# Kernel optimization log

Measured on AMD Instinct MI355X. Metric: run time of the kernel, lower is better.

## Reference

```python
import jax, jax.numpy as jnp
import numpy as np

B, T, D = 32, 2048, 512

def setup_inputs() -> dict:
    key = jax.random.key(0)
    k1, k2, k3 = jax.random.split(key, 3)
    return {
        "query": jax.random.normal(k1, (B, D), dtype=jnp.float32),
        "key": jax.random.normal(k2, (B, T, D), dtype=jnp.float32),
        "value": jax.random.normal(k3, (B, T, D), dtype=jnp.float32),
    }

def reference(query, key, value):
    # energy: [B, T] = bmm(key [B,T,D], query [B,D,1]).squeeze
    energy = jnp.einsum("btd,bd->bt", key, query)
    attention = jax.nn.softmax(energy, axis=1)  # over T, no scaling/masking (faithful)
    # context: [B, D] = bmm(attention [B,1,T], value [B,T,D]).squeeze
    out = jnp.einsum("bt,btd->bd", attention, value)
    return (out, attention)
```

## Files before the change

kernel.cpp:

```cpp
#include <hip/hip_runtime.h>

#define B_ 32
#define T_ 2048
#define D_ 512

__global__ __launch_bounds__(256) void energy_kernel(
    const float* __restrict__ q,
    const float* __restrict__ key,
    float* __restrict__ energy)
{
    __shared__ float4 qs[128];
    const int b = blockIdx.x >> 9;
    if (threadIdx.x < 128)
        qs[threadIdx.x] = ((const float4*)q)[b * 128 + threadIdx.x];
    __syncthreads();

    const int wave = threadIdx.x >> 6;
    const int lane = threadIdx.x & 63;
    const int gw   = blockIdx.x * 4 + wave;
    const int t    = gw & (T_ - 1);

    const float4* k4 = (const float4*)key + (size_t)(b * T_ + t) * (D_ / 4);
    float acc = 0.f;
#pragma unroll
    for (int j = 0; j < 2; ++j) {
        float4 kv = k4[j * 64 + lane];
        float4 qv = qs[j * 64 + lane];
        acc += kv.x * qv.x + kv.y * qv.y + kv.z * qv.z + kv.w * qv.w;
    }
#pragma unroll
    for (int off = 32; off >= 1; off >>= 1)
        acc += __shfl_down(acc, off);
    if (lane == 0)
        energy[gw] = acc;
}

__global__ __launch_bounds__(256) void softmax_kernel(
    const float* __restrict__ energy,
    float* __restrict__ attn)
{
    const int b = blockIdx.x;
    const int wave = threadIdx.x >> 6;
    const int lane = threadIdx.x & 63;

    const float4* e4 = (const float4*)(energy + b * T_);
    float4 v0 = e4[threadIdx.x * 2 + 0];
    float4 v1 = e4[threadIdx.x * 2 + 1];

    float m = fmaxf(fmaxf(fmaxf(v0.x, v0.y), fmaxf(v0.z, v0.w)),
                    fmaxf(fmaxf(v1.x, v1.y), fmaxf(v1.z, v1.w)));
#pragma unroll
    for (int off = 32; off >= 1; off >>= 1)
        m = fmaxf(m, __shfl_xor(m, off));
    __shared__ float redm[4];
    if (lane == 0) redm[wave] = m;
    __syncthreads();
    m = fmaxf(fmaxf(redm[0], redm[1]), fmaxf(redm[2], redm[3]));

    float4 x0, x1;
    x0.x = expf(v0.x - m); x0.y = expf(v0.y - m);
    x0.z = expf(v0.z - m); x0.w = expf(v0.w - m);
    x1.x = expf(v1.x - m); x1.y = expf(v1.y - m);
    x1.z = expf(v1.z - m); x1.w = expf(v1.w - m);
    float s = x0.x + x0.y + x0.z + x0.w + x1.x + x1.y + x1.z + x1.w;
#pragma unroll
    for (int off = 32; off >= 1; off >>= 1)
        s += __shfl_xor(s, off);
    __shared__ float reds[4];
    if (lane == 0) reds[wave] = s;
    __syncthreads();
    s = reds[0] + reds[1] + reds[2] + reds[3];

    const float inv = 1.f / s;
    x0.x *= inv; x0.y *= inv; x0.z *= inv; x0.w *= inv;
    x1.x *= inv; x1.y *= inv; x1.z *= inv; x1.w *= inv;

    float4* a4 = (float4*)(attn + b * T_);
    a4[threadIdx.x * 2 + 0] = x0;
    a4[threadIdx.x * 2 + 1] = x1;
}

__global__ __launch_bounds__(512) void context_partial_kernel(
    const float* __restrict__ attn,
    const float* __restrict__ value,
    float* __restrict__ partial)
{
    __shared__ float  attn_s[256];
    __shared__ float4 red4[512];

    const int b     = blockIdx.x >> 3;
    const int chunk = blockIdx.x & 7;
    const int t0    = chunk * 256;

    if (threadIdx.x < 256)
        attn_s[threadIdx.x] = attn[b * T_ + t0 + threadIdx.x];
    __syncthreads();

    const int tg = threadIdx.x >> 7;
    const int d4 = threadIdx.x & 127;

    const float4* v4 = (const float4*)value + (size_t)(b * T_ + t0 + tg) * (D_ / 4) + d4;
    float4 acc = {0.f, 0.f, 0.f, 0.f};
#pragma unroll 8
    for (int i = 0; i < 64; ++i) {
        const float a = attn_s[4 * i + tg];
        const float4 vv = v4[i * 4 * (D_ / 4)];
        acc.x += a * vv.x; acc.y += a * vv.y;
        acc.z += a * vv.z; acc.w += a * vv.w;
    }

    red4[tg * 128 + d4] = acc;
    __syncthreads();
    if (threadIdx.x < 128) {
        float4 a0 = red4[threadIdx.x +   0];
        float4 a1 = red4[threadIdx.x + 128];
        float4 a2 = red4[threadIdx.x + 256];
        float4 a3 = red4[threadIdx.x + 384];
        float4 sv;
        sv.x = a0.x + a1.x + a2.x + a3.x;
        sv.y = a0.y + a1.y + a2.y + a3.y;
        sv.z = a0.z + a1.z + a2.z + a3.z;
        sv.w = a0.w + a1.w + a2.w + a3.w;
        ((float4*)partial)[(b * 8 + chunk) * 128 + threadIdx.x] = sv;
    }
}

__global__ __launch_bounds__(128) void reduce_kernel(
    const float* __restrict__ partial,
    float* __restrict__ out)
{
    const int b  = blockIdx.x;
    const int d4 = threadIdx.x;
    float4 s = {0.f, 0.f, 0.f, 0.f};
#pragma unroll
    for (int c = 0; c < 8; ++c) {
        float4 p = ((const float4*)partial)[(b * 8 + c) * 128 + d4];
        s.x += p.x; s.y += p.y; s.z += p.z; s.w += p.w;
    }
    ((float4*)out)[b * 128 + d4] = s;
}

extern "C" void kernel_launch(void* const* d_in, const int* in_sizes, int n_in,
                              void* d_out, int out_size, void* d_ws, size_t ws_size,
                              hipStream_t stream)
{
    const float* q     = (const float*)d_in[0];
    const float* key   = (const float*)d_in[1];
    const float* value = (const float*)d_in[2];

    float* out  = (float*)d_out;
    float* attn = out + B_ * D_;

    float* energy  = (float*)d_ws;
    float* partial = energy + B_ * T_;

    energy_kernel<<<B_ * T_ / 4, 256, 0, stream>>>(q, key, energy);
    softmax_kernel<<<B_, 256, 0, stream>>>(energy, attn);
    context_partial_kernel<<<B_ * 8, 512, 0, stream>>>(attn, value, partial);
    reduce_kernel<<<B_, 128, 0, stream>>>(partial, out);
}
```

Baseline: 277.6 us.

## Rebalance energy and context kernels: more rows per wave, more context blocks

The energy kernel now has each wave handle 8 key rows, holding the query in registers instead of shared memory and dropping the block barrier, so far fewer blocks are launched. The context kernel splits T into 32 chunks of 64 with 256-thread blocks, giving 1024 blocks instead of 256 to fill more CUs while streaming value. The reduce kernel then sums 32 partials per batch instead of 8. Softmax switches to fast __expf, trading a little accuracy for cheaper exponentials.

```diff
diff --git a/kernel.cpp b/kernel.cpp
--- a/kernel.cpp
+++ b/kernel.cpp
@@ -9,30 +9,29 @@
     const float* __restrict__ key,
     float* __restrict__ energy)
 {
-    __shared__ float4 qs[128];
-    const int b = blockIdx.x >> 9;
-    if (threadIdx.x < 128)
-        qs[threadIdx.x] = ((const float4*)q)[b * 128 + threadIdx.x];
-    __syncthreads();
-
+    const int b    = blockIdx.x >> 6;
+    const int t0   = (blockIdx.x & 63) * 32;
     const int wave = threadIdx.x >> 6;
     const int lane = threadIdx.x & 63;
-    const int gw   = blockIdx.x * 4 + wave;
-    const int t    = gw & (T_ - 1);
 
-    const float4* k4 = (const float4*)key + (size_t)(b * T_ + t) * (D_ / 4);
-    float acc = 0.f;
+    const float4 qv0 = ((const float4*)q)[b * 128 + lane];
+    const float4 qv1 = ((const float4*)q)[b * 128 + 64 + lane];
+
+    const int trow = t0 + wave * 8;
+    const float4* kbase = (const float4*)key + ((size_t)b * T_ + trow) * 128;
+
+#pragma unroll 4
+    for (int r = 0; r < 8; ++r) {
+        const float4 k0 = kbase[r * 128 + lane];
+        const float4 k1 = kbase[r * 128 + 64 + lane];
+        float acc = k0.x * qv0.x + k0.y * qv0.y + k0.z * qv0.z + k0.w * qv0.w
+                  + k1.x * qv1.x + k1.y * qv1.y + k1.z * qv1.z + k1.w * qv1.w;
 #pragma unroll
-    for (int j = 0; j < 2; ++j) {
-        float4 kv = k4[j * 64 + lane];
-        float4 qv = qs[j * 64 + lane];
-        acc += kv.x * qv.x + kv.y * qv.y + kv.z * qv.z + kv.w * qv.w;
+        for (int off = 32; off >= 1; off >>= 1)
+            acc += __shfl_down(acc, off);
+        if (lane == 0)
+            energy[b * T_ + trow + r] = acc;
     }
-#pragma unroll
-    for (int off = 32; off >= 1; off >>= 1)
-        acc += __shfl_down(acc, off);
-    if (lane == 0)
-        energy[gw] = acc;
 }
 
 __global__ __launch_bounds__(256) void softmax_kernel(
@@ -58,10 +57,10 @@
     m = fmaxf(fmaxf(redm[0], redm[1]), fmaxf(redm[2], redm[3]));
 
     float4 x0, x1;
-    x0.x = expf(v0.x - m); x0.y = expf(v0.y - m);
-    x0.z = expf(v0.z - m); x0.w = expf(v0.w - m);
-    x1.x = expf(v1.x - m); x1.y = expf(v1.y - m);
-    x1.z = expf(v1.z - m); x1.w = expf(v1.w - m);
+    x0.x = __expf(v0.x - m); x0.y = __expf(v0.y - m);
+    x0.z = __expf(v0.z - m); x0.w = __expf(v0.w - m);
+    x1.x = __expf(v1.x - m); x1.y = __expf(v1.y - m);
+    x1.z = __expf(v1.z - m); x1.w = __expf(v1.w - m);
     float s = x0.x + x0.y + x0.z + x0.w + x1.x + x1.y + x1.z + x1.w;
 #pragma unroll
     for (int off = 32; off >= 1; off >>= 1)
@@ -80,48 +79,41 @@
     a4[threadIdx.x * 2 + 1] = x1;
 }
 
-__global__ __launch_bounds__(512) void context_partial_kernel(
+__global__ __launch_bounds__(256) void context_partial_kernel(
     const float* __restrict__ attn,
     const float* __restrict__ value,
     float* __restrict__ partial)
 {
-    __shared__ float  attn_s[256];
-    __shared__ float4 red4[512];
+    __shared__ float  attn_s[64];
+    __shared__ float4 red4[128];
 
-    const int b     = blockIdx.x >> 3;
-    const int chunk = blockIdx.x & 7;
-    const int t0    = chunk * 256;
+    const int b     = blockIdx.x >> 5;
+    const int chunk = blockIdx.x & 31;
+    const int t0    = chunk * 64;
 
-    if (threadIdx.x < 256)
+    if (threadIdx.x < 64)
         attn_s[threadIdx.x] = attn[b * T_ + t0 + threadIdx.x];
     __syncthreads();
 
     const int tg = threadIdx.x >> 7;
     const int d4 = threadIdx.x & 127;
 
-    const float4* v4 = (const float4*)value + (size_t)(b * T_ + t0 + tg) * (D_ / 4) + d4;
+    const float4* v4 = (const float4*)value + ((size_t)b * T_ + t0 + tg) * 128 + d4;
     float4 acc = {0.f, 0.f, 0.f, 0.f};
 #pragma unroll 8
-    for (int i = 0; i < 64; ++i) {
-        const float a = attn_s[4 * i + tg];
-        const float4 vv = v4[i * 4 * (D_ / 4)];
+    for (int i = 0; i < 32; ++i) {
+        const float a = attn_s[2 * i + tg];
+        const float4 vv = v4[i * 256];
         acc.x += a * vv.x; acc.y += a * vv.y;
         acc.z += a * vv.z; acc.w += a * vv.w;
     }
 
-    red4[tg * 128 + d4] = acc;
+    if (tg == 1) red4[d4] = acc;
     __syncthreads();
-    if (threadIdx.x < 128) {
-        float4 a0 = red4[threadIdx.x +   0];
-        float4 a1 = red4[threadIdx.x + 128];
-        float4 a2 = red4[threadIdx.x + 256];
-        float4 a3 = red4[threadIdx.x + 384];
-        float4 sv;
-        sv.x = a0.x + a1.x + a2.x + a3.x;
-        sv.y = a0.y + a1.y + a2.y + a3.y;
-        sv.z = a0.z + a1.z + a2.z + a3.z;
-        sv.w = a0.w + a1.w + a2.w + a3.w;
-        ((float4*)partial)[(b * 8 + chunk) * 128 + threadIdx.x] = sv;
+    if (tg == 0) {
+        const float4 o = red4[d4];
+        acc.x += o.x; acc.y += o.y; acc.z += o.z; acc.w += o.w;
+        ((float4*)partial)[((size_t)b * 32 + chunk) * 128 + d4] = acc;
     }
 }
 
@@ -133,8 +125,8 @@
     const int d4 = threadIdx.x;
     float4 s = {0.f, 0.f, 0.f, 0.f};
 #pragma unroll
-    for (int c = 0; c < 8; ++c) {
-        float4 p = ((const float4*)partial)[(b * 8 + c) * 128 + d4];
+    for (int c = 0; c < 32; ++c) {
+        const float4 p = ((const float4*)partial)[((size_t)b * 32 + c) * 128 + d4];
         s.x += p.x; s.y += p.y; s.z += p.z; s.w += p.w;
     }
     ((float4*)out)[b * 128 + d4] = s;
@@ -154,8 +146,8 @@
     float* energy  = (float*)d_ws;
     float* partial = energy + B_ * T_;
 
-    energy_kernel<<<B_ * T_ / 4, 256, 0, stream>>>(q, key, energy);
+    energy_kernel<<<B_ * 64, 256, 0, stream>>>(q, key, energy);
     softmax_kernel<<<B_, 256, 0, stream>>>(energy, attn);
-    context_partial_kernel<<<B_ * 8, 512, 0, stream>>>(attn, value, partial);
+    context_partial_kernel<<<B_ * 32, 256, 0, stream>>>(attn, value, partial);
     reduce_kernel<<<B_, 128, 0, stream>>>(partial, out);
 }
```

New measurement: 288.0 us. 1.04x slower.
